# Optimization experiments

Hardware: AMD Instinct MI355X
Metric: run time of the kernel (lower is better)

## Reference

```python
import jax, jax.numpy as jnp
import numpy as np

NBASE = 4                       # number of bases (DNA)
NSTATE = 2 * NBASE * (NBASE + 1)  # = 40 flip-flop transition states
SCALE = 5.0
LARGE_LOG_VAL = 50000.0


def setup_inputs() -> dict:
    key = jax.random.key(0)
    kx, kw, kb = jax.random.split(key, 3)
    T, N, INSIZE = 2048, 128, 256
    x = jax.random.normal(kx, (T, N, INSIZE), dtype=jnp.float32)
    # orthonormal-ish init approximated by scaled gaussian
    W = jax.random.normal(kw, (NSTATE, INSIZE), dtype=jnp.float32) / np.float32(np.sqrt(INSIZE))
    b = 0.5 * jax.random.normal(kb, (NSTATE,), dtype=jnp.float32)
    return {"x": x, "W": W, "b": b}


def _log_partition_flipflop(scores):
    """Forward-algorithm log partition function. scores: (T, N, C)."""
    T, N, C = scores.shape
    fwd0 = jnp.concatenate(
        [jnp.zeros((N, NBASE), scores.dtype),
         jnp.full((N, NBASE), -LARGE_LOG_VAL, scores.dtype)], axis=1)
    logZ0 = jax.nn.logsumexp(fwd0, axis=1, keepdims=True)  # (N, 1)
    fwd0 = fwd0 - logZ0

    def step(carry, scores_t):
        fwd, logZ = carry
        # (N, nbase+1, 2*nbase): to-state grouped transition scores
        curr = fwd[:, None, :] + scores_t.reshape(N, NBASE + 1, 2 * NBASE)
        base1 = jax.nn.logsumexp(curr[:, :NBASE], axis=2)            # (N, nbase) flip states
        base2 = jnp.logaddexp(curr[:, NBASE, :NBASE],
                              curr[:, NBASE, NBASE:])               # (N, nbase) flop states
        new_state = jnp.concatenate([base1, base2], axis=1)          # (N, 2*nbase)
        factors = jax.nn.logsumexp(new_state, axis=1, keepdims=True)  # (N, 1)
        return (new_state - factors, logZ + factors), None

    (_, logZ), _ = jax.lax.scan(step, (fwd0, logZ0), scores)
    return logZ  # (N, 1)


def reference(x, W, b):
    T = x.shape[0]
    # scale * tanh(x W^T + b) -> transition scores (T, N, NSTATE)
    y = SCALE * jnp.tanh(jnp.einsum('tni,ci->tnc', x, W) + b)
    logZ = _log_partition_flipflop(y)          # (N, 1)
    return y - logZ / np.float32(T)            # broadcast over T and C
```

## Files before the change

kernel.cpp:

```cpp
#include <hip/hip_runtime.h>
#include <hip/hip_bf16.h>

#define T_DIM 2048
#define N_DIM 128
#define K_DIM 256
#define C_DIM 40
#define SEG 256
#define SEGLEN 8
#define GRP 8
#define SEGPERGRP 32

typedef __attribute__((ext_vector_type(8))) short bf16x8;
typedef __attribute__((ext_vector_type(4))) float f32x4v;

__device__ __forceinline__ unsigned pack_bf16(float a, float b) {
    union { float f; unsigned u; } ua, ub;
    ua.f = a; ub.f = b;
    unsigned ra = (ua.u + 0x7FFFu + ((ua.u >> 16) & 1u)) >> 16;
    unsigned rb = (ub.u + 0x7FFFu + ((ub.u >> 16) & 1u)) >> 16;
    return (ra & 0xFFFFu) | (rb << 16);
}

__device__ __forceinline__ unsigned cvt_pk(float a, float b) {
    unsigned r;
    asm("v_cvt_pk_bf16_f32 %0, %1, %2" : "=v"(r) : "v"(a), "v"(b));
    return r;
}

__device__ __forceinline__ float bf_lo(unsigned u) {
    union { unsigned x; float f; } v; v.x = u << 16; return v.f;
}
__device__ __forceinline__ float bf_hi(unsigned u) {
    union { unsigned x; float f; } v; v.x = u & 0xFFFF0000u; return v.f;
}

__device__ __forceinline__ float fast_tanh(float v) {
    float e = __expf(2.f * v);
    return 1.f - 2.f / (e + 1.f);
}

__global__ __launch_bounds__(256, 2) void k_gemm_tanh(
    const float* __restrict__ x, const float* __restrict__ W,
    const float* __restrict__ b, unsigned* __restrict__ ybf)
{
    __shared__ __align__(16) float shX[4][2][16][128];

    const int tid = threadIdx.x;
    const int lane = tid & 63;
    const int wave = tid >> 6;
    const int lr = lane & 15;
    const int kg = lane >> 4;
    const int bid = blockIdx.x;
    const int sbid = (bid & 7) * 64 + (bid >> 3);
    const int gw = sbid * 4 + wave;

    bf16x8 wf[3][8];
    #pragma unroll
    for (int cb = 0; cb < 3; ++cb) {
        #pragma unroll
        for (int kk = 0; kk < 8; ++kk) {
            int rowc = cb * 16 + lr;
            float4 w0 = {0.f, 0.f, 0.f, 0.f}, w1 = {0.f, 0.f, 0.f, 0.f};
            if (rowc < C_DIM) {
                const float* wp = W + rowc * K_DIM + kg * 8 + kk * 32;
                w0 = *reinterpret_cast<const float4*>(wp);
                w1 = *reinterpret_cast<const float4*>(wp + 4);
            }
            union { bf16x8 v; unsigned u[4]; } uw;
            uw.u[0] = pack_bf16(w0.x, w0.y);
            uw.u[1] = pack_bf16(w0.z, w0.w);
            uw.u[2] = pack_bf16(w1.x, w1.y);
            uw.u[3] = pack_bf16(w1.z, w1.w);
            wf[cb][kk] = uw.v;
        }
    }

    float4 bia0 = *reinterpret_cast<const float4*>(b + kg * 4);
    float4 bia1 = *reinterpret_cast<const float4*>(b + 16 + kg * 4);
    float4 bia2 = {0.f, 0.f, 0.f, 0.f};
    if (kg < 2) bia2 = *reinterpret_cast<const float4*>(b + 32 + kg * 4);

    auto stage = [&](int h) {
        size_t tile = (size_t)(h >> 1) * 2048 + gw;
        const char* gbase = reinterpret_cast<const char*>(x)
                          + tile * 16384 + (h & 1) * 512;
        float* lbase = &shX[wave][h & 1][0][0];
        #pragma unroll
        for (int j = 0; j < 8; ++j) {
            int r = 2 * j + (lane >> 5);
            const void* gp = gbase + r * 1024 + (lane & 31) * 16;
            __builtin_amdgcn_global_load_lds(
                (const __attribute__((address_space(1))) void*)gp,
                (__attribute__((address_space(3))) void*)(lbase + j * 256),
                16, 0, 2 );
        }
    };

    f32x4v acc0, acc1, acc2;

#define COMPUTE_HALF(KH)                                                          \
    do {                                                                          \
        const char* cX = reinterpret_cast<const char*>(&shX[wave][KH][0][0]);     \
        _Pragma("unroll")                                                         \
        for (int kt = 0; kt < 4; ++kt) {                                          \
            int k0 = kg * 32 + kt * 128;                                          \
            float4 d0 = *reinterpret_cast<const float4*>(cX + lr * 512 + k0);      \
            float4 d1 = *reinterpret_cast<const float4*>(cX + lr * 512 + k0 + 16); \
            union { bf16x8 v; unsigned u[4]; } xf;                                \
            xf.u[0] = cvt_pk(d0.x, d0.y);                                         \
            xf.u[1] = cvt_pk(d0.z, d0.w);                                         \
            xf.u[2] = cvt_pk(d1.x, d1.y);                                         \
            xf.u[3] = cvt_pk(d1.z, d1.w);                                         \
            acc0 = __builtin_amdgcn_mfma_f32_16x16x32_bf16(wf[0][KH * 4 + kt], xf.v, acc0, 0, 0, 0); \
            acc1 = __builtin_amdgcn_mfma_f32_16x16x32_bf16(wf[1][KH * 4 + kt], xf.v, acc1, 0, 0, 0); \
            acc2 = __builtin_amdgcn_mfma_f32_16x16x32_bf16(wf[2][KH * 4 + kt], xf.v, acc2, 0, 0, 0); \
        }                                                                         \
    } while (0)

    stage(0);
    stage(1);

    for (int t = 0; t < 8; ++t) {
        __builtin_amdgcn_sched_barrier(0);
        if (t == 0) asm volatile("s_waitcnt vmcnt(8)" ::: "memory");
        else        asm volatile("s_waitcnt vmcnt(11)" ::: "memory");
        __builtin_amdgcn_sched_barrier(0);
        acc0 = (f32x4v){0.f, 0.f, 0.f, 0.f};
        acc1 = (f32x4v){0.f, 0.f, 0.f, 0.f};
        acc2 = (f32x4v){0.f, 0.f, 0.f, 0.f};
        COMPUTE_HALF(0);
        __builtin_amdgcn_sched_barrier(0);
        if (t < 7) stage(2 * t + 2);

        __builtin_amdgcn_sched_barrier(0);
        if (t < 7) asm volatile("s_waitcnt vmcnt(8)" ::: "memory");
        else       asm volatile("s_waitcnt vmcnt(0)" ::: "memory");
        __builtin_amdgcn_sched_barrier(0);
        COMPUTE_HALF(1);

        size_t row = ((size_t)t * 2048 + gw) * 16 + lr;
        unsigned* yr = ybf + row * 20;
        float o00 = 5.f * fast_tanh(acc0[0] + bia0.x);
        float o01 = 5.f * fast_tanh(acc0[1] + bia0.y);
        float o02 = 5.f * fast_tanh(acc0[2] + bia0.z);
        float o03 = 5.f * fast_tanh(acc0[3] + bia0.w);
        float o10 = 5.f * fast_tanh(acc1[0] + bia1.x);
        float o11 = 5.f * fast_tanh(acc1[1] + bia1.y);
        float o12 = 5.f * fast_tanh(acc1[2] + bia1.z);
        float o13 = 5.f * fast_tanh(acc1[3] + bia1.w);
        uint2 p0, p1;
        p0.x = cvt_pk(o00, o01); p0.y = cvt_pk(o02, o03);
        p1.x = cvt_pk(o10, o11); p1.y = cvt_pk(o12, o13);
        *reinterpret_cast<uint2*>(yr + kg * 2) = p0;
        *reinterpret_cast<uint2*>(yr + 8 + kg * 2) = p1;
        if (kg < 2) {
            float o20 = 5.f * fast_tanh(acc2[0] + bia2.x);
            float o21 = 5.f * fast_tanh(acc2[1] + bia2.y);
            float o22 = 5.f * fast_tanh(acc2[2] + bia2.z);
            float o23 = 5.f * fast_tanh(acc2[3] + bia2.w);
            uint2 p2;
            p2.x = cvt_pk(o20, o21); p2.y = cvt_pk(o22, o23);
            *reinterpret_cast<uint2*>(yr + 16 + kg * 2) = p2;
        }

        __builtin_amdgcn_sched_barrier(0);
        if (t < 7) stage(2 * t + 3);
    }
#undef COMPUTE_HALF
}

__global__ __launch_bounds__(128) void k_seg(
    const unsigned* __restrict__ ybf, float* __restrict__ segv, float* __restrict__ segl)
{
    int tid = blockIdx.x * 128 + threadIdx.x;
    int n = tid & 127;
    int s = tid >> 7;

    float P[8][8];
    #pragma unroll
    for (int j = 0; j < 8; ++j)
        #pragma unroll
        for (int c = 0; c < 8; ++c) P[j][c] = (j == c) ? 1.f : 0.f;

    for (int st = 0; st < SEGLEN; ++st) {
        int t = s * SEGLEN + st;
        const unsigned* yr = ybf + ((size_t)t * N_DIM + n) * 20;
        float e[40];
        #pragma unroll
        for (int i = 0; i < 5; ++i) {
            uint4 w = reinterpret_cast<const uint4*>(yr)[i];
            e[i * 8 + 0] = __expf(bf_lo(w.x));
            e[i * 8 + 1] = __expf(bf_hi(w.x));
            e[i * 8 + 2] = __expf(bf_lo(w.y));
            e[i * 8 + 3] = __expf(bf_hi(w.y));
            e[i * 8 + 4] = __expf(bf_lo(w.z));
            e[i * 8 + 5] = __expf(bf_hi(w.z));
            e[i * 8 + 6] = __expf(bf_lo(w.w));
            e[i * 8 + 7] = __expf(bf_hi(w.w));
        }
        #pragma unroll
        for (int c = 0; c < 8; ++c) {
            float np[8];
            #pragma unroll
            for (int j = 0; j < 4; ++j) {
                float a = 0.f;
                #pragma unroll
                for (int i = 0; i < 8; ++i) a += P[i][c] * e[j * 8 + i];
                np[j] = a;
            }
            #pragma unroll
            for (int j = 0; j < 4; ++j)
                np[4 + j] = P[j][c] * e[32 + j] + P[4 + j][c] * e[36 + j];
            #pragma unroll
            for (int j = 0; j < 8; ++j) P[j][c] = np[j];
        }
    }
    #pragma unroll
    for (int c = 0; c < 8; ++c) {
        float sum = 0.f;
        #pragma unroll
        for (int j = 0; j < 8; ++j) sum += P[j][c];
        float inv = 1.f / sum;
        #pragma unroll
        for (int j = 0; j < 8; ++j)
            segv[(((size_t)s * 8 + c) * 8 + j) * N_DIM + n] = P[j][c] * inv;
        segl[((size_t)s * 8 + c) * N_DIM + n] = __logf(sum);
    }
}

__global__ __launch_bounds__(128) void k_grp(
    const float* __restrict__ segv, const float* __restrict__ segl,
    float* __restrict__ grpv, float* __restrict__ grpl)
{
    int tid = blockIdx.x * 128 + threadIdx.x;
    int n = tid & 127;
    int cc = (tid >> 7) & 7;
    int g = tid >> 10;

    float u[8];
    #pragma unroll
    for (int i = 0; i < 8; ++i) u[i] = (i == cc) ? 1.f : 0.f;
    float logacc = 0.f;

    for (int s = g * SEGPERGRP; s < (g + 1) * SEGPERGRP; ++s) {
        float l[8];
        #pragma unroll
        for (int i = 0; i < 8; ++i) l[i] = segl[((size_t)s * 8 + i) * N_DIM + n];
        float m = l[0];
        #pragma unroll
        for (int i = 1; i < 8; ++i) m = fmaxf(m, l[i]);
        float nu[8] = {0.f, 0.f, 0.f, 0.f, 0.f, 0.f, 0.f, 0.f};
        #pragma unroll
        for (int i = 0; i < 8; ++i) {
            float wi = u[i] * __expf(l[i] - m);
            #pragma unroll
            for (int j = 0; j < 8; ++j)
                nu[j] += wi * segv[(((size_t)s * 8 + i) * 8 + j) * N_DIM + n];
        }
        float sum = 0.f;
        #pragma unroll
        for (int j = 0; j < 8; ++j) sum += nu[j];
        float inv = 1.f / sum;
        #pragma unroll
        for (int j = 0; j < 8; ++j) u[j] = nu[j] * inv;
        logacc += m + __logf(sum);
    }
    #pragma unroll
    for (int j = 0; j < 8; ++j)
        grpv[(((size_t)g * 8 + cc) * 8 + j) * N_DIM + n] = u[j];
    grpl[((size_t)g * 8 + cc) * N_DIM + n] = logacc;
}

__global__ void k_fin(const float* __restrict__ grpv, const float* __restrict__ grpl,
                      float* __restrict__ lz)
{
    int n = threadIdx.x;
    float p[8] = {0.25f, 0.25f, 0.25f, 0.25f, 0.f, 0.f, 0.f, 0.f};
    float logZ = 1.3862943611198906f;

    for (int g = 0; g < GRP; ++g) {
        float l[8];
        #pragma unroll
        for (int i = 0; i < 8; ++i) l[i] = grpl[((size_t)g * 8 + i) * N_DIM + n];
        float m = l[0];
        #pragma unroll
        for (int i = 1; i < 8; ++i) m = fmaxf(m, l[i]);
        float nu[8] = {0.f, 0.f, 0.f, 0.f, 0.f, 0.f, 0.f, 0.f};
        #pragma unroll
        for (int i = 0; i < 8; ++i) {
            float wi = p[i] * __expf(l[i] - m);
            #pragma unroll
            for (int j = 0; j < 8; ++j)
                nu[j] += wi * grpv[(((size_t)g * 8 + i) * 8 + j) * N_DIM + n];
        }
        float sum = 0.f;
        #pragma unroll
        for (int j = 0; j < 8; ++j) sum += nu[j];
        float inv = 1.f / sum;
        #pragma unroll
        for (int j = 0; j < 8; ++j) p[j] = nu[j] * inv;
        logZ += m + __logf(sum);
    }
    lz[n] = logZ * (1.f / (float)T_DIM);
}

__global__ __launch_bounds__(256) void k_sub(const unsigned* __restrict__ ybf,
                                             const float* __restrict__ lz,
                                             float* __restrict__ out)
{
    int i = blockIdx.x * 256 + threadIdx.x;
    int n = (i / 10) & 127;
    float d = lz[n];
    uint2 w = *reinterpret_cast<const uint2*>(ybf + 2 * (size_t)i);
    float4 v;
    v.x = bf_lo(w.x) - d;
    v.y = bf_hi(w.x) - d;
    v.z = bf_lo(w.y) - d;
    v.w = bf_hi(w.y) - d;
    reinterpret_cast<float4*>(out)[i] = v;
}

extern "C" void kernel_launch(void* const* d_in, const int* in_sizes, int n_in,
                              void* d_out, int out_size, void* d_ws, size_t ws_size,
                              hipStream_t stream) {
    const float* x = (const float*)d_in[0];
    const float* W = (const float*)d_in[1];
    const float* b = (const float*)d_in[2];
    float* out = (float*)d_out;
    float* ws = (float*)d_ws;

    unsigned* ybf = (unsigned*)ws;
    float* segv = ws + 5242880;
    float* segl = ws + 7340032;
    float* grpv = ws + 7602176;
    float* grpl = ws + 7667712;
    float* lz   = ws + 7675904;

    k_gemm_tanh<<<512, 256, 0, stream>>>(x, W, b, ybf);
    k_seg<<<256, 128, 0, stream>>>(ybf, segv, segl);
    k_grp<<<64, 128, 0, stream>>>(segv, segl, grpv, grpl);
    k_fin<<<1, 128, 0, stream>>>(grpv, grpl, lz);
    k_sub<<<10240, 256, 0, stream>>>(ybf, lz, out);
}
```

Baseline: 137.9 us.

## Convert x to bf16 in registers before LDS staging with swizzled block-shared tiles

Replaces the per-wave direct global-to-LDS fp32 staging with block-cooperative coalesced float4 loads into registers. These are converted to bf16 and written into a double-buffered, XOR-swizzled shared tile, so the MFMA loop reads one 16-byte bf16 fragment per k-step. This halves LDS footprint and read traffic, drops the per-wave conversions inside the compute loop, and avoids bank conflicts. In exchange it holds many more registers for in-flight loads, needs a block-wide barrier every iteration, and loses the async global_load_lds overlap.

```diff
diff --git a/kernel.cpp b/kernel.cpp
--- a/kernel.cpp
+++ b/kernel.cpp
@@ -43,7 +43,7 @@
     const float* __restrict__ x, const float* __restrict__ W,
     const float* __restrict__ b, unsigned* __restrict__ ybf)
 {
-    __shared__ __align__(16) float shX[4][2][16][128];
+    __shared__ __align__(16) uint2 shX[2][64][64];
 
     const int tid = threadIdx.x;
     const int lane = tid & 63;
@@ -52,7 +52,7 @@
     const int kg = lane >> 4;
     const int bid = blockIdx.x;
     const int sbid = (bid & 7) * 64 + (bid >> 3);
-    const int gw = sbid * 4 + wave;
+    char* lds = reinterpret_cast<char*>(&shX[0][0][0]);
 
     bf16x8 wf[3][8];
     #pragma unroll
@@ -80,65 +80,60 @@
     float4 bia2 = {0.f, 0.f, 0.f, 0.f};
     if (kg < 2) bia2 = *reinterpret_cast<const float4*>(b + 32 + kg * 4);
 
-    auto stage = [&](int h) {
-        size_t tile = (size_t)(h >> 1) * 2048 + gw;
-        const char* gbase = reinterpret_cast<const char*>(x)
-                          + tile * 16384 + (h & 1) * 512;
-        float* lbase = &shX[wave][h & 1][0][0];
-        #pragma unroll
-        for (int j = 0; j < 8; ++j) {
-            int r = 2 * j + (lane >> 5);
-            const void* gp = gbase + r * 1024 + (lane & 31) * 16;
-            __builtin_amdgcn_global_load_lds(
-                (const __attribute__((address_space(1))) void*)gp,
-                (__attribute__((address_space(3))) void*)(lbase + j * 256),
-                16, 0, 2 );
+    const float4* x4 = reinterpret_cast<const float4*>(x);
+    uint2 st[16];
+
+    auto LOADCVT = [&](int i) {
+        size_t base = ((size_t)i * 512 + sbid) * 4096;
+        float4 v[16];
+        #pragma unroll
+        for (int j = 0; j < 16; ++j)
+            v[j] = x4[base + j * 256 + tid];
+        #pragma unroll
+        for (int j = 0; j < 16; ++j) {
+            st[j].x = cvt_pk(v[j].x, v[j].y);
+            st[j].y = cvt_pk(v[j].z, v[j].w);
         }
     };
 
-    f32x4v acc0, acc1, acc2;
-
-#define COMPUTE_HALF(KH)                                                          \
-    do {                                                                          \
-        const char* cX = reinterpret_cast<const char*>(&shX[wave][KH][0][0]);     \
-        _Pragma("unroll")                                                         \
-        for (int kt = 0; kt < 4; ++kt) {                                          \
-            int k0 = kg * 32 + kt * 128;                                          \
-            float4 d0 = *reinterpret_cast<const float4*>(cX + lr * 512 + k0);      \
-            float4 d1 = *reinterpret_cast<const float4*>(cX + lr * 512 + k0 + 16); \
-            union { bf16x8 v; unsigned u[4]; } xf;                                \
-            xf.u[0] = cvt_pk(d0.x, d0.y);                                         \
-            xf.u[1] = cvt_pk(d0.z, d0.w);                                         \
-            xf.u[2] = cvt_pk(d1.x, d1.y);                                         \
-            xf.u[3] = cvt_pk(d1.z, d1.w);                                         \
-            acc0 = __builtin_amdgcn_mfma_f32_16x16x32_bf16(wf[0][KH * 4 + kt], xf.v, acc0, 0, 0, 0); \
-            acc1 = __builtin_amdgcn_mfma_f32_16x16x32_bf16(wf[1][KH * 4 + kt], xf.v, acc1, 0, 0, 0); \
-            acc2 = __builtin_amdgcn_mfma_f32_16x16x32_bf16(wf[2][KH * 4 + kt], xf.v, acc2, 0, 0, 0); \
-        }                                                                         \
-    } while (0)
-
-    stage(0);
-    stage(1);
-
-    for (int t = 0; t < 8; ++t) {
+    auto WRITE = [&](int d) {
+        #pragma unroll
+        for (int j = 0; j < 16; ++j) {
+            int r = 4 * j + wave;
+            char* p = lds + d * 32768 + r * 512 + ((lane * 8) ^ ((r & 7) << 4));
+            *reinterpret_cast<uint2*>(p) = st[j];
+        }
+    };
+
+    for (int i0 = 0; i0 < 1; ++i0) {
+        LOADCVT(0);
+        WRITE(0);
+        LOADCVT(1);
+        asm volatile("s_waitcnt lgkmcnt(0)" ::: "memory");
+        __builtin_amdgcn_s_barrier();
         __builtin_amdgcn_sched_barrier(0);
-        if (t == 0) asm volatile("s_waitcnt vmcnt(8)" ::: "memory");
-        else        asm volatile("s_waitcnt vmcnt(11)" ::: "memory");
-        __builtin_amdgcn_sched_barrier(0);
-        acc0 = (f32x4v){0.f, 0.f, 0.f, 0.f};
-        acc1 = (f32x4v){0.f, 0.f, 0.f, 0.f};
-        acc2 = (f32x4v){0.f, 0.f, 0.f, 0.f};
-        COMPUTE_HALF(0);
-        __builtin_amdgcn_sched_barrier(0);
-        if (t < 7) stage(2 * t + 2);
-
-        __builtin_amdgcn_sched_barrier(0);
-        if (t < 7) asm volatile("s_waitcnt vmcnt(8)" ::: "memory");
-        else       asm volatile("s_waitcnt vmcnt(0)" ::: "memory");
-        __builtin_amdgcn_sched_barrier(0);
-        COMPUTE_HALF(1);
-
-        size_t row = ((size_t)t * 2048 + gw) * 16 + lr;
+    }
+
+    for (int i = 0; i < 8; ++i) {
+        int cur = i & 1;
+        if (i < 7) WRITE(cur ^ 1);
+        if (i < 6) LOADCVT(i + 2);
+
+        f32x4v acc0 = {0.f, 0.f, 0.f, 0.f};
+        f32x4v acc1 = {0.f, 0.f, 0.f, 0.f};
+        f32x4v acc2 = {0.f, 0.f, 0.f, 0.f};
+        const char* rbase = lds + cur * 32768 + (wave * 16 + lr) * 512;
+        const int swz = (lr & 7) << 4;
+        #pragma unroll
+        for (int kt = 0; kt < 8; ++kt) {
+            bf16x8 xf = *reinterpret_cast<const bf16x8*>(
+                rbase + ((kt * 64 + kg * 16) ^ swz));
+            acc0 = __builtin_amdgcn_mfma_f32_16x16x32_bf16(wf[0][kt], xf, acc0, 0, 0, 0);
+            acc1 = __builtin_amdgcn_mfma_f32_16x16x32_bf16(wf[1][kt], xf, acc1, 0, 0, 0);
+            acc2 = __builtin_amdgcn_mfma_f32_16x16x32_bf16(wf[2][kt], xf, acc2, 0, 0, 0);
+        }
+
+        size_t row = ((size_t)i * 512 + sbid) * 64 + wave * 16 + lr;
         unsigned* yr = ybf + row * 20;
         float o00 = 5.f * fast_tanh(acc0[0] + bia0.x);
         float o01 = 5.f * fast_tanh(acc0[1] + bia0.y);
@@ -163,10 +158,10 @@
             *reinterpret_cast<uint2*>(yr + 16 + kg * 2) = p2;
         }
 
+        asm volatile("s_waitcnt lgkmcnt(0)" ::: "memory");
+        __builtin_amdgcn_s_barrier();
         __builtin_amdgcn_sched_barrier(0);
-        if (t < 7) stage(2 * t + 3);
-    }
-#undef COMPUTE_HALF
+    }
 }
 
 __global__ __launch_bounds__(128) void k_seg(
```

Measured after the change: 143.9 us. +4.3%, slower.

## Deepen GEMM LDS prefetch pipeline from two to four half-tile stages

Applied to the files above, without the earlier changes.

The GEMM+tanh kernel's per-wave LDS staging buffer grows from 2 to 4 half-tile slots. The loop is restructured to process one half-tile per iteration, with four stages in flight and vmcnt waits adjusted to match. This keeps more global loads outstanding to hide memory latency. In exchange, LDS use doubles to 128KB per block, so launch bounds drop to one block per CU, which lowers occupancy.

```diff
diff --git a/kernel.cpp b/kernel.cpp
--- a/kernel.cpp
+++ b/kernel.cpp
@@ -39,11 +39,11 @@
     return 1.f - 2.f / (e + 1.f);
 }
 
-__global__ __launch_bounds__(256, 2) void k_gemm_tanh(
+__global__ __launch_bounds__(256, 1) void k_gemm_tanh(
     const float* __restrict__ x, const float* __restrict__ W,
     const float* __restrict__ b, unsigned* __restrict__ ybf)
 {
-    __shared__ __align__(16) float shX[4][2][16][128];
+    __shared__ __align__(16) float shX[4][4][16][128];
 
     const int tid = threadIdx.x;
     const int lane = tid & 63;
@@ -84,7 +84,7 @@
         size_t tile = (size_t)(h >> 1) * 2048 + gw;
         const char* gbase = reinterpret_cast<const char*>(x)
                           + tile * 16384 + (h & 1) * 512;
-        float* lbase = &shX[wave][h & 1][0][0];
+        float* lbase = &shX[wave][h & 3][0][0];
         #pragma unroll
         for (int j = 0; j < 8; ++j) {
             int r = 2 * j + (lane >> 5);
@@ -98,9 +98,9 @@
 
     f32x4v acc0, acc1, acc2;
 
-#define COMPUTE_HALF(KH)                                                          \
+#define COMPUTE_HALF(BUF, KH)                                                     \
     do {                                                                          \
-        const char* cX = reinterpret_cast<const char*>(&shX[wave][KH][0][0]);     \
+        const char* cX = reinterpret_cast<const char*>(BUF);                      \
         _Pragma("unroll")                                                         \
         for (int kt = 0; kt < 4; ++kt) {                                          \
             int k0 = kg * 32 + kt * 128;                                          \
@@ -119,52 +119,59 @@
 
     stage(0);
     stage(1);
-
-    for (int t = 0; t < 8; ++t) {
+    stage(2);
+    stage(3);
+
+    for (int j = 0; j < 16; ++j) {
         __builtin_amdgcn_sched_barrier(0);
-        if (t == 0) asm volatile("s_waitcnt vmcnt(8)" ::: "memory");
-        else        asm volatile("s_waitcnt vmcnt(11)" ::: "memory");
+        if (j >= 4 && j <= 12)      asm volatile("s_waitcnt vmcnt(30)" ::: "memory");
+        else if (j < 2)             asm volatile("s_waitcnt vmcnt(24)" ::: "memory");
+        else if (j < 4)             asm volatile("s_waitcnt vmcnt(27)" ::: "memory");
+        else if (j == 13)           asm volatile("s_waitcnt vmcnt(22)" ::: "memory");
+        else if (j == 14)           asm volatile("s_waitcnt vmcnt(14)" ::: "memory");
+        else                        asm volatile("s_waitcnt vmcnt(6)"  ::: "memory");
         __builtin_amdgcn_sched_barrier(0);
-        acc0 = (f32x4v){0.f, 0.f, 0.f, 0.f};
-        acc1 = (f32x4v){0.f, 0.f, 0.f, 0.f};
-        acc2 = (f32x4v){0.f, 0.f, 0.f, 0.f};
-        COMPUTE_HALF(0);
+
+        if ((j & 1) == 0) {
+            acc0 = (f32x4v){0.f, 0.f, 0.f, 0.f};
+            acc1 = (f32x4v){0.f, 0.f, 0.f, 0.f};
+            acc2 = (f32x4v){0.f, 0.f, 0.f, 0.f};
+            COMPUTE_HALF(&shX[wave][j & 3][0][0], 0);
+        } else {
+            COMPUTE_HALF(&shX[wave][j & 3][0][0], 1);
+        }
         __builtin_amdgcn_sched_barrier(0);
-        if (t < 7) stage(2 * t + 2);
-
+
+        if (j < 12) stage(j + 4);
+
+        if (j & 1) {
+            int t = j >> 1;
+            size_t row = ((size_t)t * 2048 + gw) * 16 + lr;
+            unsigned* yr = ybf + row * 20;
+            float o00 = 5.f * fast_tanh(acc0[0] + bia0.x);
+            float o01 = 5.f * fast_tanh(acc0[1] + bia0.y);
+            float o02 = 5.f * fast_tanh(acc0[2] + bia0.z);
+            float o03 = 5.f * fast_tanh(acc0[3] + bia0.w);
+            float o10 = 5.f * fast_tanh(acc1[0] + bia1.x);
+            float o11 = 5.f * fast_tanh(acc1[1] + bia1.y);
+            float o12 = 5.f * fast_tanh(acc1[2] + bia1.z);
+            float o13 = 5.f * fast_tanh(acc1[3] + bia1.w);
+            uint2 p0, p1;
+            p0.x = cvt_pk(o00, o01); p0.y = cvt_pk(o02, o03);
+            p1.x = cvt_pk(o10, o11); p1.y = cvt_pk(o12, o13);
+            *reinterpret_cast<uint2*>(yr + kg * 2) = p0;
+            *reinterpret_cast<uint2*>(yr + 8 + kg * 2) = p1;
+            if (kg < 2) {
+                float o20 = 5.f * fast_tanh(acc2[0] + bia2.x);
+                float o21 = 5.f * fast_tanh(acc2[1] + bia2.y);
+                float o22 = 5.f * fast_tanh(acc2[2] + bia2.z);
+                float o23 = 5.f * fast_tanh(acc2[3] + bia2.w);
+                uint2 p2;
+                p2.x = cvt_pk(o20, o21); p2.y = cvt_pk(o22, o23);
+                *reinterpret_cast<uint2*>(yr + 16 + kg * 2) = p2;
+            }
+        }
         __builtin_amdgcn_sched_barrier(0);
-        if (t < 7) asm volatile("s_waitcnt vmcnt(8)" ::: "memory");
-        else       asm volatile("s_waitcnt vmcnt(0)" ::: "memory");
-        __builtin_amdgcn_sched_barrier(0);
-        COMPUTE_HALF(1);
-
-        size_t row = ((size_t)t * 2048 + gw) * 16 + lr;
-        unsigned* yr = ybf + row * 20;
-        float o00 = 5.f * fast_tanh(acc0[0] + bia0.x);
-        float o01 = 5.f * fast_tanh(acc0[1] + bia0.y);
-        float o02 = 5.f * fast_tanh(acc0[2] + bia0.z);
-        float o03 = 5.f * fast_tanh(acc0[3] + bia0.w);
-        float o10 = 5.f * fast_tanh(acc1[0] + bia1.x);
-        float o11 = 5.f * fast_tanh(acc1[1] + bia1.y);
-        float o12 = 5.f * fast_tanh(acc1[2] + bia1.z);
-        float o13 = 5.f * fast_tanh(acc1[3] + bia1.w);
-        uint2 p0, p1;
-        p0.x = cvt_pk(o00, o01); p0.y = cvt_pk(o02, o03);
-        p1.x = cvt_pk(o10, o11); p1.y = cvt_pk(o12, o13);
-        *reinterpret_cast<uint2*>(yr + kg * 2) = p0;
-        *reinterpret_cast<uint2*>(yr + 8 + kg * 2) = p1;
-        if (kg < 2) {
-            float o20 = 5.f * fast_tanh(acc2[0] + bia2.x);
-            float o21 = 5.f * fast_tanh(acc2[1] + bia2.y);
-            float o22 = 5.f * fast_tanh(acc2[2] + bia2.z);
-            float o23 = 5.f * fast_tanh(acc2[3] + bia2.w);
-            uint2 p2;
-            p2.x = cvt_pk(o20, o21); p2.y = cvt_pk(o22, o23);
-            *reinterpret_cast<uint2*>(yr + 16 + kg * 2) = p2;
-        }
-
-        __builtin_amdgcn_sched_barrier(0);
-        if (t < 7) stage(2 * t + 3);
     }
 #undef COMPUTE_HALF
 }
```

Result: slower. 148.6 us (+7.8%).
